# Kernel tuning notes

Measured on AMD Instinct MI355X. Metric: run time of the kernel, lower is better.

The kernel has to match this reference:

```python
import jax, jax.numpy as jnp
import numpy as np

N, NFEAT, NHID, NCLASS, NHEADS = 8192, 512, 64, 16, 4
ALPHA = 0.2          # leaky_relu slope for attention scores
OUT_SLOPE = 0.01     # flax default slope for per-head output leaky_relu
NEG = -9000000000000000.0


def glorot(key, shape):
    fan_in, fan_out = shape[0], shape[1]
    lim = jnp.sqrt(6.0 / (fan_in + fan_out))
    return jax.random.uniform(key, shape, jnp.float32, -lim, lim)


def setup_inputs() -> dict:
    key = jax.random.key(0)
    ks = jax.random.split(key, 6)
    x = jax.random.normal(ks[0], (N, NFEAT), jnp.float32)
    adj = jax.random.randint(ks[1], (N, N), 0, 2, jnp.int32)
    Wh = glorot(ks[2], (NHEADS * NFEAT, NHID)).reshape(NHEADS, NFEAT, NHID)
    ah = glorot(ks[3], (NHEADS * 2 * NHID, 1)).reshape(NHEADS, 2 * NHID, 1)
    Wo = glorot(ks[4], (NHID * NHEADS, NCLASS))
    ao = glorot(ks[5], (2 * NCLASS, 1))
    return {"x": x, "adj": adj, "Wh": Wh, "ah": ah, "Wo": Wo, "ao": ao}


def _gat_layer(x, adj_mask, W, a, score_slope):
    # h: (N, F)
    h = x @ W
    F = h.shape[1]
    # a_input[i,j] = concat(h_i, h_j); a_input @ a == f1[i] + f2[j]
    f1 = h @ a[:F, 0]   # (N,)
    f2 = h @ a[F:, 0]   # (N,)
    e = jax.nn.leaky_relu(f1[:, None] + f2[None, :], negative_slope=score_slope)
    att = jax.nn.softmax(jnp.where(adj_mask, e, NEG), axis=1)  # (N, N)
    return att @ h  # (N, F)


def reference(x, adj, Wh, ah, Wo, ao):
    adj_mask = adj > 0
    heads = []
    for k in range(NHEADS):  # small fixed structural loop
        hp = _gat_layer(x, adj_mask, Wh[k], ah[k], ALPHA)
        heads.append(jax.nn.leaky_relu(hp, negative_slope=OUT_SLOPE))
    xcat = jnp.concatenate(heads, axis=1)  # (N, NHEADS*NHID)
    # output head: concat=False -> return h_prime directly
    return _gat_layer(xcat, adj_mask, Wo, ao, ALPHA)  # (N, NCLASS)
```

## Files before the change

kernel.cpp:

```cpp
#include <hip/hip_runtime.h>
#include <stdint.h>

#define N      8192
#define NW32   256
#define FEAT   512
#define HID    64
#define NH     4
#define C1     256
#define PCH    65
#define TC     260
#define NCLS   16
#define C2     32
#define IPB    8
#define LOG2E  1.44269504f

typedef __attribute__((ext_vector_type(8))) short bf16x8;
typedef __attribute__((ext_vector_type(4))) float f32x4;

__device__ __forceinline__ float b2f(uint16_t u){
  uint32_t x = ((uint32_t)u) << 16;
  return __builtin_bit_cast(float, x);
}
__device__ __forceinline__ uint16_t f2b(float f){
  uint32_t x = __builtin_bit_cast(uint32_t, f);
  uint32_t r = (x + 0x7fffu + ((x >> 16) & 1u)) >> 16;
  return (uint16_t)r;
}
__device__ __forceinline__ float lrelu(float v, float a){ return fmaxf(v, a * v); }
__device__ __forceinline__ float fexp2(float x){
#if __has_builtin(__builtin_amdgcn_exp2f)
  return __builtin_amdgcn_exp2f(x);
#else
  return exp2f(x);
#endif
}
__device__ __forceinline__ uint32_t pk_bf16(float lo, float hi){
  uint32_t r;
  asm("v_cvt_pk_bf16_f32 %0, %1, %2" : "=v"(r) : "v"(lo), "v"(hi));
  return r;
}

__device__ __forceinline__ bf16x8 mk_frag(float f1v, float4 fa, float4 fb,
                                          uint32_t ub, float& dsum){
  float e0, e1, e2, e3, e4, e5, e6, e7, s;
  s = f1v + fa.x; e0 = fexp2(fmaxf(s, 0.2f * s)); if (!(ub &   1u)) e0 = 0.f;
  s = f1v + fa.y; e1 = fexp2(fmaxf(s, 0.2f * s)); if (!(ub &   2u)) e1 = 0.f;
  s = f1v + fa.z; e2 = fexp2(fmaxf(s, 0.2f * s)); if (!(ub &   4u)) e2 = 0.f;
  s = f1v + fa.w; e3 = fexp2(fmaxf(s, 0.2f * s)); if (!(ub &   8u)) e3 = 0.f;
  s = f1v + fb.x; e4 = fexp2(fmaxf(s, 0.2f * s)); if (!(ub &  16u)) e4 = 0.f;
  s = f1v + fb.y; e5 = fexp2(fmaxf(s, 0.2f * s)); if (!(ub &  32u)) e5 = 0.f;
  s = f1v + fb.z; e6 = fexp2(fmaxf(s, 0.2f * s)); if (!(ub &  64u)) e6 = 0.f;
  s = f1v + fb.w; e7 = fexp2(fmaxf(s, 0.2f * s)); if (!(ub & 128u)) e7 = 0.f;
  dsum += ((e0 + e1) + (e2 + e3)) + ((e4 + e5) + (e6 + e7));
  union { uint32_t u[4]; bf16x8 v; } r;
  r.u[0] = pk_bf16(e0, e1);
  r.u[1] = pk_bf16(e2, e3);
  r.u[2] = pk_bf16(e4, e5);
  r.u[3] = pk_bf16(e6, e7);
  return r.v;
}

__global__ __launch_bounds__(256) void kp_pack(const int* __restrict__ adj,
                                               unsigned long long* __restrict__ adjP64){
  int t = threadIdx.x;
  int lane = t & 63;
  int wg = blockIdx.x * 4 + (t >> 6);
  for (int it = 0; it < 128; ++it){
    size_t c = (size_t)it * 8192 + wg;
    int v = adj[c * 64 + lane];
    unsigned long long m = __ballot(v > 0);
    if (lane == 0) adjP64[c] = m;
  }
}

__global__ void k0_wht(const float* __restrict__ Wh, float* __restrict__ WhT){
  int idx = blockIdx.x * 256 + threadIdx.x;
  int k = idx >> 15;
  int r = idx & 32767;
  int cc = r >> 9, f = r & 511;
  WhT[idx] = Wh[k * 32768 + f * 64 + cc];
}

__global__ __launch_bounds__(256) void k1_h(const float* __restrict__ x,
    const float* __restrict__ WhT, const float* __restrict__ ah,
    uint16_t* __restrict__ H, float* __restrict__ f1, float* __restrict__ f2)
{
  __shared__ float4 xs[IPB][128];
  int t = threadIdx.x;
  int i0 = blockIdx.x * IPB;
  for (int r = t; r < IPB * 128; r += 256){
    int ii = r >> 7, o = r & 127;
    xs[ii][o] = *((const float4*)(x + (size_t)(i0 + ii) * FEAT) + o);
  }
  __syncthreads();
  int k = t >> 6, cc = t & 63;
  const float4* wrow = (const float4*)(WhT + k * 32768 + cc * 512);
  float acc[IPB] = {};
  for (int f4 = 0; f4 < 128; ++f4){
    float4 wv = wrow[f4];
    #pragma unroll
    for (int ii = 0; ii < IPB; ++ii){
      float4 xv = xs[ii][f4];
      acc[ii] += xv.x * wv.x + xv.y * wv.y + xv.z * wv.z + xv.w * wv.w;
    }
  }
  float a1 = ah[k * 128 + cc], a2 = ah[k * 128 + 64 + cc];
  #pragma unroll
  for (int ii = 0; ii < IPB; ++ii){
    int i = i0 + ii;
    H[(size_t)i * C1 + t] = f2b(acc[ii]);
    float c1v = acc[ii] * a1, c2v = acc[ii] * a2;
    #pragma unroll
    for (int off = 32; off; off >>= 1){
      c1v += __shfl_down(c1v, off);
      c2v += __shfl_down(c2v, off);
    }
    if (cc == 0){ f1[k * N + i] = c1v * LOG2E; f2[k * N + i] = c2v * LOG2E; }
  }
}

__global__ void k2a_htT(const uint16_t* __restrict__ H, uint16_t* __restrict__ HT){
  __shared__ uint16_t tile[64][65];
  int bid = blockIdx.x;
  int k = bid & 3, it = bid >> 2;
  int i0 = it * 64;
  int t = threadIdx.x;
  #pragma unroll
  for (int r = 0; r < 4; ++r){
    int ii = r * 16 + (t >> 4);
    int pp = (t & 15) * 4;
    uint2 v = *(const uint2*)(H + (size_t)(i0 + ii) * C1 + k * 64 + pp);
    const uint16_t* s = (const uint16_t*)&v;
    tile[pp + 0][ii] = s[0]; tile[pp + 1][ii] = s[1];
    tile[pp + 2][ii] = s[2]; tile[pp + 3][ii] = s[3];
  }
  __syncthreads();
  #pragma unroll
  for (int r = 0; r < 4; ++r){
    int pp = r * 16 + (t >> 4);
    int ii = (t & 15) * 4;
    uint2 v;
    uint16_t* s = (uint16_t*)&v;
    s[0] = tile[pp][ii + 0]; s[1] = tile[pp][ii + 1];
    s[2] = tile[pp][ii + 2]; s[3] = tile[pp][ii + 3];
    *(uint2*)(HT + (size_t)k * (64 * N) + (size_t)pp * N + i0 + ii) = v;
  }
}

#define K3_BODY(JC, CUR, NXT)                                                   \
  {                                                                             \
    const int gjn = js * 2048 + (((JC) + 1) & 63) * 32;                         \
    _Pragma("unroll")                                                           \
    for (int ct = 0; ct < 4; ++ct)                                              \
      b##NXT[ct] = *(const bf16x8*)(hbase + (size_t)ct * 16 * N + gjn);         \
    w##NXT##0 = adjP[arow0 + (gjn >> 5)];                                       \
    w##NXT##1 = adjP[arow1 + (gjn >> 5)];                                       \
    f##NXT##0 = *(const float4*)(f2h + gjn + 8 * q);                            \
    f##NXT##1 = *(const float4*)(f2h + gjn + 8 * q + 4);                        \
    bf16x8 af0 = mk_frag(f1v0, f##CUR##0, f##CUR##1,                            \
                         (w##CUR##0 >> (8 * q)) & 255u, dsum0);                 \
    bf16x8 af1 = mk_frag(f1v1, f##CUR##0, f##CUR##1,                            \
                         (w##CUR##1 >> (8 * q)) & 255u, dsum1);                 \
    _Pragma("unroll")                                                           \
    for (int ct = 0; ct < 4; ++ct){                                             \
      acc[0][ct] = __builtin_amdgcn_mfma_f32_16x16x32_bf16(af0, b##CUR[ct], acc[0][ct], 0, 0, 0); \
      acc[1][ct] = __builtin_amdgcn_mfma_f32_16x16x32_bf16(af1, b##CUR[ct], acc[1][ct], 0, 0, 0); \
    }                                                                           \
  }

__global__ __launch_bounds__(256, 4) void k3_attA(const uint32_t* __restrict__ adjP,
    const uint16_t* __restrict__ HT, const float* __restrict__ f1,
    const float* __restrict__ f2, float* __restrict__ accA)
{
  const int t = threadIdx.x;
  const int ibl = blockIdx.x & 255;
  const int js  = blockIdx.x >> 8;
  const int gi0 = ibl * 32;

  const int lane = t & 63;
  const int head = t >> 6;
  const int m    = lane & 15;
  const int q    = lane >> 4;

  const int row0  = gi0 + m;
  const int arow0 = row0 * NW32;
  const int arow1 = (row0 + 16) * NW32;
  const float* f2h = f2 + (size_t)head * N;
  const float f1v0 = f1[(size_t)head * N + row0];
  const float f1v1 = f1[(size_t)head * N + row0 + 16];
  const uint16_t* hbase = HT + (size_t)(head * 64 + m) * N + 8 * q;

  f32x4 acc[2][4] = {};
  float dsum0 = 0.f, dsum1 = 0.f;

  bf16x8 bA[4], bB[4];
  uint32_t wA0, wA1, wB0, wB1;
  float4 fA0, fA1, fB0, fB1;

  {
    const int gj0 = js * 2048;
    #pragma unroll
    for (int ct = 0; ct < 4; ++ct)
      bA[ct] = *(const bf16x8*)(hbase + (size_t)ct * 16 * N + gj0);
    wA0 = adjP[arow0 + (gj0 >> 5)];
    wA1 = adjP[arow1 + (gj0 >> 5)];
    fA0 = *(const float4*)(f2h + gj0 + 8 * q);
    fA1 = *(const float4*)(f2h + gj0 + 8 * q + 4);
  }

  for (int jc = 0; jc < 64; jc += 2){
    K3_BODY(jc,     A, B)
    K3_BODY(jc + 1, B, A)
  }

  #pragma unroll
  for (int itl = 0; itl < 2; ++itl)
    #pragma unroll
    for (int ct = 0; ct < 4; ++ct)
      #pragma unroll
      for (int reg = 0; reg < 4; ++reg){
        int gi = gi0 + itl * 16 + q * 4 + reg;
        accA[((size_t)js * N + gi) * TC + head * PCH + ct * 16 + m] = acc[itl][ct][reg];
      }
  {
    float v0 = dsum0, v1 = dsum1;
    v0 += __shfl_xor(v0, 16); v0 += __shfl_xor(v0, 32);
    v1 += __shfl_xor(v1, 16); v1 += __shfl_xor(v1, 32);
    if (q == 0){
      accA[((size_t)js * N + row0)      * TC + head * PCH + 64] = v0;
      accA[((size_t)js * N + row0 + 16) * TC + head * PCH + 64] = v1;
    }
  }
}

__global__ void k4_redA(const float* __restrict__ accA, uint16_t* __restrict__ xcat){
  int i = blockIdx.x;
  int t = threadIdx.x;
  int k = t >> 6, cc = t & 63;
  size_t base = (size_t)i * TC + k * PCH;
  float v = 0.f, Z = 0.f;
  #pragma unroll
  for (int js = 0; js < 4; ++js){
    const float* p = accA + (size_t)js * N * TC + base;
    v += p[cc];
    Z += p[64];
  }
  float r = v / Z;
  xcat[(size_t)i * C1 + t] = f2b(lrelu(r, 0.01f));
}

__global__ __launch_bounds__(256) void k5_h2(const uint16_t* __restrict__ xcat,
    const float* __restrict__ Wo, const float* __restrict__ ao,
    uint16_t* __restrict__ h2T, float* __restrict__ f1o, float* __restrict__ f2o)
{
  __shared__ uint16_t xs[16][256];
  int t = threadIdx.x;
  int i0 = blockIdx.x * 16;
  #pragma unroll
  for (int r = 0; r < 2; ++r){
    int idx = t + 256 * r;
    int ii = idx >> 5, o4 = idx & 31;
    *(uint4*)&xs[ii][o4 * 8] = *(const uint4*)(xcat + (size_t)(i0 + ii) * C1 + o4 * 8);
  }
  __syncthreads();
  int ii = t >> 4, c = t & 15;
  float acc = 0.f;
  for (int f = 0; f < 256; ++f)
    acc += b2f(xs[ii][f]) * Wo[f * 16 + c];
  int i = i0 + ii;
  h2T[(size_t)c * N + i] = f2b(acc);
  float u1 = acc * ao[c];
  float u2 = acc * ao[16 + c];
  #pragma unroll
  for (int off = 8; off; off >>= 1){
    u1 += __shfl_down(u1, off, 16);
    u2 += __shfl_down(u2, off, 16);
  }
  if (c == 0){ f1o[i] = u1 * LOG2E; f2o[i] = u2 * LOG2E; }
}

#define K6_BODY(JC, CUR, NXT)                                                   \
  {                                                                             \
    const int gjn = js * 1024 + (((JC) + 1) & 31) * 32;                         \
    b##NXT = *(const bf16x8*)(hbase + gjn);                                     \
    w##NXT = adjP[arow + (gjn >> 5)];                                           \
    f##NXT##0 = *(const float4*)(f2o + gjn + 8 * q);                            \
    f##NXT##1 = *(const float4*)(f2o + gjn + 8 * q + 4);                        \
    bf16x8 af = mk_frag(f1v, f##CUR##0, f##CUR##1,                              \
                        (w##CUR >> (8 * q)) & 255u, dsum);                      \
    acc0 = __builtin_amdgcn_mfma_f32_16x16x32_bf16(af, b##CUR, acc0, 0, 0, 0);  \
  }

__global__ __launch_bounds__(256, 4) void k6_attB(const uint32_t* __restrict__ adjP,
    const uint16_t* __restrict__ h2T, const float* __restrict__ f1o,
    const float* __restrict__ f2o, float* __restrict__ accB)
{
  const int t = threadIdx.x;
  const int ibl = blockIdx.x & 127;
  const int js  = blockIdx.x >> 7;
  const int gi0 = ibl * 64;

  const int lane = t & 63;
  const int w = t >> 6;
  const int m = lane & 15;
  const int q = lane >> 4;

  const int row = gi0 + w * 16 + m;
  const int arow = row * NW32;
  const float f1v = f1o[row];
  const uint16_t* hbase = h2T + (size_t)m * N + 8 * q;

  f32x4 acc0 = {0.f, 0.f, 0.f, 0.f};
  float dsum = 0.f;

  bf16x8 bA, bB;
  uint32_t wA, wB;
  float4 fA0, fA1, fB0, fB1;

  {
    const int gj0 = js * 1024;
    bA = *(const bf16x8*)(hbase + gj0);
    wA = adjP[arow + (gj0 >> 5)];
    fA0 = *(const float4*)(f2o + gj0 + 8 * q);
    fA1 = *(const float4*)(f2o + gj0 + 8 * q + 4);
  }

  for (int jc = 0; jc < 32; jc += 2){
    K6_BODY(jc,     A, B)
    K6_BODY(jc + 1, B, A)
  }

  #pragma unroll
  for (int reg = 0; reg < 4; ++reg){
    int gi = gi0 + w * 16 + q * 4 + reg;
    accB[((size_t)js * N + gi) * C2 + m] = acc0[reg];
  }
  {
    float v = dsum;
    v += __shfl_xor(v, 16); v += __shfl_xor(v, 32);
    if (q == 0)
      accB[((size_t)js * N + row) * C2 + 16] = v;
  }
}

__global__ void k7_redB(const float* __restrict__ accB, float* __restrict__ out){
  int idx = blockIdx.x * 256 + threadIdx.x;
  int i = idx >> 4, c = idx & 15;
  float v = 0.f, Z = 0.f;
  #pragma unroll
  for (int js = 0; js < 8; ++js){
    const float* p = accB + ((size_t)js * N + i) * C2;
    v += p[c];
    Z += p[16];
  }
  out[idx] = v / Z;
}

extern "C" void kernel_launch(void* const* d_in, const int* in_sizes, int n_in,
                              void* d_out, int out_size, void* d_ws, size_t ws_size,
                              hipStream_t stream)
{
  const float* x   = (const float*)d_in[0];
  const int*   adj = (const int*)d_in[1];
  const float* Wh  = (const float*)d_in[2];
  const float* ah  = (const float*)d_in[3];
  const float* Wo  = (const float*)d_in[4];
  const float* ao  = (const float*)d_in[5];
  float* out = (float*)d_out;

  char* ws = (char*)d_ws;
  float*    WhT  = (float*)   (ws);
  uint16_t* H    = (uint16_t*)(ws + 524288);
  uint16_t* HT   = (uint16_t*)(ws + 4718592);
  float*    f1   = (float*)   (ws + 8912896);
  float*    f2   = (float*)   (ws + 9043968);
  float*    accA = (float*)   (ws + 9175040);
  uint16_t* xcat = (uint16_t*)(ws + 43253760);
  uint16_t* h2T  = (uint16_t*)(ws + 47448064);
  float*    f1o  = (float*)   (ws + 47710208);
  float*    f2o  = (float*)   (ws + 47742976);
  float*    accB = (float*)   (ws + 47775744);
  void*     adjP = (void*)    (ws + 56164352);

  hipLaunchKernelGGL(kp_pack,  dim3(2048), dim3(256), 0, stream, adj, (unsigned long long*)adjP);
  hipLaunchKernelGGL(k0_wht,   dim3(512),  dim3(256), 0, stream, Wh, WhT);
  hipLaunchKernelGGL(k1_h,     dim3(1024), dim3(256), 0, stream, x, WhT, ah, H, f1, f2);
  hipLaunchKernelGGL(k2a_htT,  dim3(512),  dim3(256), 0, stream, H, HT);
  hipLaunchKernelGGL(k3_attA,  dim3(1024), dim3(256), 0, stream, (const uint32_t*)adjP, HT, f1, f2, accA);
  hipLaunchKernelGGL(k4_redA,  dim3(8192), dim3(256), 0, stream, accA, xcat);
  hipLaunchKernelGGL(k5_h2,    dim3(512),  dim3(256), 0, stream, xcat, Wo, ao, h2T, f1o, f2o);
  hipLaunchKernelGGL(k6_attB,  dim3(1024), dim3(256), 0, stream, (const uint32_t*)adjP, h2T, f1o, f2o, accB);
  hipLaunchKernelGGL(k7_redB,  dim3(512),  dim3(256), 0, stream, accB, out);
}
```

Baseline: 716.6 us.

## Pre-pack B operands into MFMA fragment order for fully coalesced loads

The transpose kernel and the output-projection kernel now write H and h2 directly in the per-lane MFMA B-fragment layout, so each wavefront's B loads in the attention kernels become contiguous 16-byte reads per lane. Before, each lane's B fragment came from a strided row of the transposed array, spreading one wavefront's load over many rows. The packing kernels take on more index arithmetic, and k5 adds shared-memory staging plus a barrier.

```diff
diff --git a/kernel.cpp b/kernel.cpp
--- a/kernel.cpp
+++ b/kernel.cpp
@@ -119,8 +119,8 @@
   }
 }
 
-__global__ void k2a_htT(const uint16_t* __restrict__ H, uint16_t* __restrict__ HT){
-  __shared__ uint16_t tile[64][65];
+__global__ void k2a_pack(const uint16_t* __restrict__ H, uint16_t* __restrict__ Bp){
+  __shared__ uint16_t tile[64][72];
   int bid = blockIdx.x;
   int k = bid & 3, it = bid >> 2;
   int i0 = it * 64;
@@ -136,23 +136,24 @@
   }
   __syncthreads();
   #pragma unroll
-  for (int r = 0; r < 4; ++r){
-    int pp = r * 16 + (t >> 4);
-    int ii = (t & 15) * 4;
-    uint2 v;
-    uint16_t* s = (uint16_t*)&v;
-    s[0] = tile[pp][ii + 0]; s[1] = tile[pp][ii + 1];
-    s[2] = tile[pp][ii + 2]; s[3] = tile[pp][ii + 3];
-    *(uint2*)(HT + (size_t)k * (64 * N) + (size_t)pp * N + i0 + ii) = v;
+  for (int r = 0; r < 2; ++r){
+    int jl = r;
+    int ct = t >> 6;
+    int lane = t & 63;
+    int m = lane & 15, q = lane >> 4;
+    uint4 v = *(const uint4*)&tile[ct * 16 + m][jl * 32 + q * 8];
+    size_t off = ((((size_t)k * 256 + (i0 >> 5) + jl) * 4 + ct) * 64 + lane) * 8;
+    *(uint4*)(Bp + off) = v;
   }
 }
 
 #define K3_BODY(JC, CUR, NXT)                                                   \
   {                                                                             \
-    const int gjn = js * 2048 + (((JC) + 1) & 63) * 32;                         \
+    const int jcn = ((JC) + 1) & 63;                                            \
+    const int gjn = js * 2048 + jcn * 32;                                       \
     _Pragma("unroll")                                                           \
     for (int ct = 0; ct < 4; ++ct)                                              \
-      b##NXT[ct] = *(const bf16x8*)(hbase + (size_t)ct * 16 * N + gjn);         \
+      b##NXT[ct] = *(const bf16x8*)(bpbase + (size_t)(jcn * 4 + ct) * 512);     \
     w##NXT##0 = adjP[arow0 + (gjn >> 5)];                                       \
     w##NXT##1 = adjP[arow1 + (gjn >> 5)];                                       \
     f##NXT##0 = *(const float4*)(f2h + gjn + 8 * q);                            \
@@ -169,7 +170,7 @@
   }
 
 __global__ __launch_bounds__(256, 4) void k3_attA(const uint32_t* __restrict__ adjP,
-    const uint16_t* __restrict__ HT, const float* __restrict__ f1,
+    const uint16_t* __restrict__ Bp, const float* __restrict__ f1,
     const float* __restrict__ f2, float* __restrict__ accA)
 {
   const int t = threadIdx.x;
@@ -188,7 +189,7 @@
   const float* f2h = f2 + (size_t)head * N;
   const float f1v0 = f1[(size_t)head * N + row0];
   const float f1v1 = f1[(size_t)head * N + row0 + 16];
-  const uint16_t* hbase = HT + (size_t)(head * 64 + m) * N + 8 * q;
+  const uint16_t* bpbase = Bp + (((size_t)head * 256 + js * 64) * 4) * 512 + lane * 8;
 
   f32x4 acc[2][4] = {};
   float dsum0 = 0.f, dsum1 = 0.f;
@@ -201,7 +202,7 @@
     const int gj0 = js * 2048;
     #pragma unroll
     for (int ct = 0; ct < 4; ++ct)
-      bA[ct] = *(const bf16x8*)(hbase + (size_t)ct * 16 * N + gj0);
+      bA[ct] = *(const bf16x8*)(bpbase + (size_t)ct * 512);
     wA0 = adjP[arow0 + (gj0 >> 5)];
     wA1 = adjP[arow1 + (gj0 >> 5)];
     fA0 = *(const float4*)(f2h + gj0 + 8 * q);
@@ -251,9 +252,10 @@
 
 __global__ __launch_bounds__(256) void k5_h2(const uint16_t* __restrict__ xcat,
     const float* __restrict__ Wo, const float* __restrict__ ao,
-    uint16_t* __restrict__ h2T, float* __restrict__ f1o, float* __restrict__ f2o)
+    uint16_t* __restrict__ Bp2, float* __restrict__ f1o, float* __restrict__ f2o)
 {
   __shared__ uint16_t xs[16][256];
+  __shared__ uint16_t hs[16][16];
   int t = threadIdx.x;
   int i0 = blockIdx.x * 16;
   #pragma unroll
@@ -268,7 +270,7 @@
   for (int f = 0; f < 256; ++f)
     acc += b2f(xs[ii][f]) * Wo[f * 16 + c];
   int i = i0 + ii;
-  h2T[(size_t)c * N + i] = f2b(acc);
+  hs[ii][c] = f2b(acc);
   float u1 = acc * ao[c];
   float u2 = acc * ao[16 + c];
   #pragma unroll
@@ -277,12 +279,23 @@
     u2 += __shfl_down(u2, off, 16);
   }
   if (c == 0){ f1o[i] = u1 * LOG2E; f2o[i] = u2 * LOG2E; }
+  __syncthreads();
+  if (t < 32){
+    int q_l = t >> 4, mm = t & 15;
+    uint16_t tmp[8];
+    #pragma unroll
+    for (int s = 0; s < 8; ++s) tmp[s] = hs[8 * q_l + s][mm];
+    int jcg = i0 >> 5, half = (i0 >> 4) & 1;
+    size_t off = ((size_t)jcg * 64 + (2 * half + q_l) * 16 + mm) * 8;
+    *(uint4*)(Bp2 + off) = *(uint4*)tmp;
+  }
 }
 
 #define K6_BODY(JC, CUR, NXT)                                                   \
   {                                                                             \
-    const int gjn = js * 1024 + (((JC) + 1) & 31) * 32;                         \
-    b##NXT = *(const bf16x8*)(hbase + gjn);                                     \
+    const int jcn = ((JC) + 1) & 31;                                            \
+    const int gjn = js * 1024 + jcn * 32;                                       \
+    b##NXT = *(const bf16x8*)(bp2 + (size_t)jcn * 512);                         \
     w##NXT = adjP[arow + (gjn >> 5)];                                           \
     f##NXT##0 = *(const float4*)(f2o + gjn + 8 * q);                            \
     f##NXT##1 = *(const float4*)(f2o + gjn + 8 * q + 4);                        \
@@ -292,7 +305,7 @@
   }
 
 __global__ __launch_bounds__(256, 4) void k6_attB(const uint32_t* __restrict__ adjP,
-    const uint16_t* __restrict__ h2T, const float* __restrict__ f1o,
+    const uint16_t* __restrict__ Bp2, const float* __restrict__ f1o,
     const float* __restrict__ f2o, float* __restrict__ accB)
 {
   const int t = threadIdx.x;
@@ -308,7 +321,7 @@
   const int row = gi0 + w * 16 + m;
   const int arow = row * NW32;
   const float f1v = f1o[row];
-  const uint16_t* hbase = h2T + (size_t)m * N + 8 * q;
+  const uint16_t* bp2 = Bp2 + ((size_t)js * 32 * 64) * 8 + lane * 8;
 
   f32x4 acc0 = {0.f, 0.f, 0.f, 0.f};
   float dsum = 0.f;
@@ -319,7 +332,7 @@
 
   {
     const int gj0 = js * 1024;
-    bA = *(const bf16x8*)(hbase + gj0);
+    bA = *(const bf16x8*)(bp2);
     wA = adjP[arow + (gj0 >> 5)];
     fA0 = *(const float4*)(f2o + gj0 + 8 * q);
     fA1 = *(const float4*)(f2o + gj0 + 8 * q + 4);
@@ -371,12 +384,12 @@
   char* ws = (char*)d_ws;
   float*    WhT  = (float*)   (ws);
   uint16_t* H    = (uint16_t*)(ws + 524288);
-  uint16_t* HT   = (uint16_t*)(ws + 4718592);
+  uint16_t* Bp   = (uint16_t*)(ws + 4718592);
   float*    f1   = (float*)   (ws + 8912896);
   float*    f2   = (float*)   (ws + 9043968);
   float*    accA = (float*)   (ws + 9175040);
   uint16_t* xcat = (uint16_t*)(ws + 43253760);
-  uint16_t* h2T  = (uint16_t*)(ws + 47448064);
+  uint16_t* Bp2  = (uint16_t*)(ws + 47448064);
   float*    f1o  = (float*)   (ws + 47710208);
   float*    f2o  = (float*)   (ws + 47742976);
   float*    accB = (float*)   (ws + 47775744);
@@ -385,10 +398,10 @@
   hipLaunchKernelGGL(kp_pack,  dim3(2048), dim3(256), 0, stream, adj, (unsigned long long*)adjP);
   hipLaunchKernelGGL(k0_wht,   dim3(512),  dim3(256), 0, stream, Wh, WhT);
   hipLaunchKernelGGL(k1_h,     dim3(1024), dim3(256), 0, stream, x, WhT, ah, H, f1, f2);
-  hipLaunchKernelGGL(k2a_htT,  dim3(512),  dim3(256), 0, stream, H, HT);
-  hipLaunchKernelGGL(k3_attA,  dim3(1024), dim3(256), 0, stream, (const uint32_t*)adjP, HT, f1, f2, accA);
+  hipLaunchKernelGGL(k2a_pack, dim3(512),  dim3(256), 0, stream, H, Bp);
+  hipLaunchKernelGGL(k3_attA,  dim3(1024), dim3(256), 0, stream, (const uint32_t*)adjP, Bp, f1, f2, accA);
   hipLaunchKernelGGL(k4_redA,  dim3(8192), dim3(256), 0, stream, accA, xcat);
-  hipLaunchKernelGGL(k5_h2,    dim3(512),  dim3(256), 0, stream, xcat, Wo, ao, h2T, f1o, f2o);
-  hipLaunchKernelGGL(k6_attB,  dim3(1024), dim3(256), 0, stream, (const uint32_t*)adjP, h2T, f1o, f2o, accB);
+  hipLaunchKernelGGL(k5_h2,    dim3(512),  dim3(256), 0, stream, xcat, Wo, ao, Bp2, f1o, f2o);
+  hipLaunchKernelGGL(k6_attB,  dim3(1024), dim3(256), 0, stream, (const uint32_t*)adjP, Bp2, f1o, f2o, accB);
   hipLaunchKernelGGL(k7_redB,  dim3(512),  dim3(256), 0, stream, accB, out);
 }
```

After: 629.8 us. -12.1%, faster.
